# Kernel optimization log

Hardware: AMD Instinct MI355X
Metric: run time of the kernel (lower is better)

## Reference

```python
import jax, jax.numpy as jnp
import numpy as np

BN_EPS = 1e-5
BIND_CHAN = 4  # hparams.MODEL.LEARNABLE_OFFSET.BIND_CHAN


def conv1x1(x, w, b):
    # x: [B,C,H,W], w: [O,C], b: [O]
    return jnp.einsum('bchw,oc->bohw', x, w) + b[None, :, None, None]


def bn_train(x, gamma, beta):
    # training-mode batch norm over (B,H,W) per channel
    mean = jnp.mean(x, axis=(0, 2, 3), keepdims=True)
    var = jnp.var(x, axis=(0, 2, 3), keepdims=True)
    xn = (x - mean) * jax.lax.rsqrt(var + BN_EPS)
    return xn * gamma[None, :, None, None] + beta[None, :, None, None]


def displace_channel(x, offsets):
    # x: [B,C,H,W]; offsets: [C,2] (dy,dx) per channel, continuous.
    # out[b,c,y,x] = bilinear sample of x[b,c] at (y+dy_c, x+dx_c), zeros outside.
    B, C, H, W = x.shape
    dy, dx = offsets[:, 0], offsets[:, 1]
    fy, fx = jnp.floor(dy), jnp.floor(dx)
    wy, wx = dy - fy, dx - fx          # fractional weights, [C]
    iy, ix = fy.astype(jnp.int32), fx.astype(jnp.int32)
    chan = jnp.arange(C)[:, None, None]

    def shifted(oy, ox):
        ys = jnp.arange(H)[None, :] + oy[:, None]   # [C,H]
        xs = jnp.arange(W)[None, :] + ox[:, None]   # [C,W]
        valid = ((ys >= 0) & (ys < H))[:, :, None] & ((xs >= 0) & (xs < W))[:, None, :]
        ysc = jnp.clip(ys, 0, H - 1)
        xsc = jnp.clip(xs, 0, W - 1)
        g = x[:, chan, ysc[:, :, None], xsc[:, None, :]]   # [B,C,H,W]
        return g * valid.astype(x.dtype)[None]

    w00 = ((1 - wy) * (1 - wx))[None, :, None, None]
    w01 = ((1 - wy) * wx)[None, :, None, None]
    w10 = (wy * (1 - wx))[None, :, None, None]
    w11 = (wy * wx)[None, :, None, None]
    return (w00 * shifted(iy, ix) + w01 * shifted(iy, ix + 1)
            + w10 * shifted(iy + 1, ix) + w11 * shifted(iy + 1, ix + 1))


def setup_inputs() -> dict:
    key = jax.random.key(0)
    ks = jax.random.split(key, 12)
    B, Cin, H, W = 16, 64, 128, 128
    Cd, Cout = 128, 64
    n_off = Cd // BIND_CHAN  # 32
    s_in = 1.0 / np.sqrt(Cin)
    s_d = 1.0 / np.sqrt(Cd)
    return {
        'x': jax.random.normal(ks[0], (B, Cin, H, W), jnp.float32),
        'pre_w': jax.random.uniform(ks[1], (Cd, Cin), jnp.float32, -s_in, s_in),
        'pre_b': jax.random.uniform(ks[2], (Cd,), jnp.float32, -s_in, s_in),
        'post_w': jax.random.uniform(ks[3], (Cout, Cd), jnp.float32, -s_d, s_d),
        'post_b': jax.random.uniform(ks[4], (Cout,), jnp.float32, -s_d, s_d),
        'atten_w': jax.random.uniform(ks[5], (Cd, Cin), jnp.float32, -s_in, s_in),
        'atten_b': jax.random.uniform(ks[6], (Cd,), jnp.float32, -s_in, s_in),
        'atten_bn_g': jnp.ones((Cd,), jnp.float32),
        'atten_bn_b': jnp.zeros((Cd,), jnp.float32),
        'offsets': jax.random.normal(ks[7], (n_off, 2), jnp.float32) * 3.0,
        'bn_g': jnp.ones((Cout,), jnp.float32),
        'bn_b': jnp.zeros((Cout,), jnp.float32),
    }


def reference(x, pre_w, pre_b, post_w, post_b, atten_w, atten_b,
              atten_bn_g, atten_bn_b, offsets, bn_g, bn_b):
    # pre_offset conv1x1
    out_pre = conv1x1(x, pre_w, pre_b)                        # [B,Cd,H,W]
    # DisplaceChannel: each offset shared by BIND_CHAN consecutive channels
    off_per_chan = jnp.repeat(offsets, BIND_CHAN, axis=0)     # [Cd,2]
    out_dis = displace_channel(out_pre, off_per_chan)
    # Attention branch: conv1x1 -> BN -> Softplus -> SpaceNormalization
    a = conv1x1(x, atten_w, atten_b)
    a = bn_train(a, atten_bn_g, atten_bn_b)
    a = jax.nn.softplus(a)
    out_atten = a / jnp.sum(a, axis=(2, 3), keepdims=True)    # spatial normalization
    # post_offset conv1x1 on gated displaced features
    out_post = conv1x1(out_atten * out_dis, post_w, post_b)
    # residual (inplanes == outplanes, stride 1 -> no downsample) + BN + ReLU
    out_skip = x + out_post
    return jax.nn.relu(bn_train(out_skip, bn_g, bn_b))
```

## Files before the change

kernel.cpp:

```cpp
#include <hip/hip_runtime.h>

#define HWSZ   16384
#define CIN    64
#define CD     128
#define COUT   64
#define BN_EPS 1e-5f

typedef __attribute__((ext_vector_type(8))) short short8x;
typedef __attribute__((ext_vector_type(4))) float floatx4;

#define WS_WT1   0
#define WS_WTP   16384
#define WS_DISP  24576
#define WS_ASTAT 25344
#define WS_OSTAT 25600
#define WS_SPAT  25728
#define WS_BIG   32768
#define WS_TOTAL_BYTES ((size_t)(32768 + 16777216) * 4)

__device__ __forceinline__ unsigned short f2bf(float f) {
    unsigned int u = __float_as_uint(f);
    u += 0x7fff + ((u >> 16) & 1);
    return (unsigned short)(u >> 16);
}
__device__ __forceinline__ float bf2f(unsigned short s) {
    return __uint_as_float(((unsigned int)s) << 16);
}
__device__ __forceinline__ float softplus_fast(float x) {
    return fmaxf(x, 0.f) + __logf(1.f + __expf(-fabsf(x)));
}
__device__ __forceinline__ float block_reduce(float v, float* sc) {
    #pragma unroll
    for (int off = 32; off >= 1; off >>= 1) v += __shfl_xor(v, off, 64);
    int wv = threadIdx.x >> 6, ln = threadIdx.x & 63;
    if (ln == 0) sc[wv] = v;
    __syncthreads();
    float r = (threadIdx.x < 4) ? sc[threadIdx.x] : 0.f;
    r += __shfl_xor(r, 1, 64);
    r += __shfl_xor(r, 2, 64);
    return r;
}

__global__ __launch_bounds__(256) void prep_kernel(
        const float* __restrict__ pre_w, const float* __restrict__ atten_w,
        const float* __restrict__ post_w, const float* __restrict__ offsets,
        float* __restrict__ ws) {
    int tid = blockIdx.x * 256 + threadIdx.x;
    unsigned short* wAB = (unsigned short*)(ws + WS_WT1);
    unsigned short* wP  = (unsigned short*)(ws + WS_WTP);
    float* disp = ws + WS_DISP;
    if (tid < 16384) {
        int o = tid >> 6, c = tid & 63;
        float v = (o < 128) ? pre_w[o * 64 + c] : atten_w[(o - 128) * 64 + c];
        wAB[tid] = f2bf(v);
    } else if (tid < 24576) {
        int k = tid - 16384;
        int o = k >> 7, c = k & 127;
        wP[k] = f2bf(post_w[o * 128 + c]);
    } else if (tid < 24704) {
        int c = tid - 24576;
        float dy = offsets[(c >> 2) * 2 + 0];
        float dx = offsets[(c >> 2) * 2 + 1];
        float fy = floorf(dy), fx = floorf(dx);
        float wy = dy - fy, wx = dx - fx;
        float* d = disp + c * 6;
        d[0] = fy; d[1] = fx;
        d[2] = (1.f - wy) * (1.f - wx);
        d[3] = (1.f - wy) * wx;
        d[4] = wy * (1.f - wx);
        d[5] = wy * wx;
    }
}

__global__ __launch_bounds__(256) void conv_pre_mfma(
        const float* __restrict__ x, const unsigned short* __restrict__ wAB,
        const float* __restrict__ pre_b, const float* __restrict__ atten_b,
        unsigned short* __restrict__ out_pre, unsigned short* __restrict__ a_out) {
    __shared__ unsigned short xT[2][64 * 72];
    int t = threadIdx.x;
    int wv = t >> 6, ln = t & 63;
    int b = blockIdx.x >> 6;
    int poff = (blockIdx.x & 63) << 8;
    const float* xg = x + (size_t)b * CIN * HWSZ + poff;
    int c = ln;

    int o0 = wv * 64;
    short8x wfrag[4][2];
    #pragma unroll
    for (int oi = 0; oi < 4; ++oi)
        #pragma unroll
        for (int kk = 0; kk < 2; ++kk) {
            int row = o0 + oi * 16 + (ln & 15);
            int kcol = kk * 32 + (ln >> 4) * 8;
            wfrag[oi][kk] = *(const short8x*)(wAB + row * 64 + kcol);
        }
    float4 biasv[4];
    #pragma unroll
    for (int oi = 0; oi < 4; ++oi) {
        int og = o0 + oi * 16;
        const float* bias = (og < 128) ? (pre_b + og) : (atten_b + og - 128);
        biasv[oi] = *(const float4*)(bias + (ln >> 4) * 4);
    }

    float4 ld[4];
    #pragma unroll
    for (int k = 0; k < 4; ++k)
        ld[k] = *(const float4*)(xg + (size_t)c * HWSZ + 0 * 64 + wv * 16 + k * 4);
    #pragma unroll
    for (int k = 0; k < 4; ++k) {
        int px = wv * 16 + k * 4;
        xT[0][(px + 0) * 72 + c] = f2bf(ld[k].x);
        xT[0][(px + 1) * 72 + c] = f2bf(ld[k].y);
        xT[0][(px + 2) * 72 + c] = f2bf(ld[k].z);
        xT[0][(px + 3) * 72 + c] = f2bf(ld[k].w);
    }
    __syncthreads();

    #pragma unroll
    for (int tt = 0; tt < 4; ++tt) {
        if (tt < 3) {
            #pragma unroll
            for (int k = 0; k < 4; ++k)
                ld[k] = *(const float4*)(xg + (size_t)c * HWSZ + (tt + 1) * 64 + wv * 16 + k * 4);
        }
        const unsigned short* buf = xT[tt & 1];
        floatx4 acc[4][4];
        #pragma unroll
        for (int oi = 0; oi < 4; ++oi)
            #pragma unroll
            for (int pi = 0; pi < 4; ++pi)
                acc[oi][pi] = floatx4{biasv[oi].x, biasv[oi].y, biasv[oi].z, biasv[oi].w};
        #pragma unroll
        for (int kk = 0; kk < 2; ++kk)
            #pragma unroll
            for (int pi = 0; pi < 4; ++pi) {
                short8x xfrag = *(const short8x*)((const char*)buf +
                        (pi * 16 + (ln & 15)) * 144 + (kk * 32 + (ln >> 4) * 8) * 2);
                #pragma unroll
                for (int oi = 0; oi < 4; ++oi)
                    acc[oi][pi] = __builtin_amdgcn_mfma_f32_16x16x32_bf16(
                            wfrag[oi][kk], xfrag, acc[oi][pi], 0, 0, 0);
            }
        int ptile = poff + tt * 64;
        #pragma unroll
        for (int oi = 0; oi < 4; ++oi) {
            int og = o0 + oi * 16;
            unsigned short* dst = (og < 128) ? out_pre : a_out;
            int ob = (og < 128) ? og : og - 128;
            #pragma unroll
            for (int pi = 0; pi < 4; ++pi) {
                int px = ptile + pi * 16 + (ln & 15);
                #pragma unroll
                for (int r = 0; r < 4; ++r) {
                    int o = ob + (ln >> 4) * 4 + r;
                    dst[((size_t)b * CD + o) * HWSZ + px] = f2bf(acc[oi][pi][r]);
                }
            }
        }
        if (tt < 3) {
            unsigned short* wbuf = xT[(tt + 1) & 1];
            #pragma unroll
            for (int k = 0; k < 4; ++k) {
                int px = wv * 16 + k * 4;
                wbuf[(px + 0) * 72 + c] = f2bf(ld[k].x);
                wbuf[(px + 1) * 72 + c] = f2bf(ld[k].y);
                wbuf[(px + 2) * 72 + c] = f2bf(ld[k].z);
                wbuf[(px + 3) * 72 + c] = f2bf(ld[k].w);
            }
        }
        __syncthreads();
    }
}

__global__ __launch_bounds__(256) void chan_stats_bf16(
        const unsigned short* __restrict__ src, float* __restrict__ stats) {
    __shared__ float sc1[8], sc2[8];
    int c = blockIdx.x, b = blockIdx.y;
    const unsigned short* base = src + ((size_t)b * CD + c) * HWSZ;
    int t = threadIdx.x;
    float sum = 0.f, sq = 0.f;
    #pragma unroll
    for (int i = 0; i < 8; ++i) {
        uint4 v = *(const uint4*)(base + i * 2048 + t * 8);
        unsigned int u[4] = {v.x, v.y, v.z, v.w};
        #pragma unroll
        for (int k = 0; k < 4; ++k) {
            float lo = bf2f((unsigned short)(u[k] & 0xffff));
            float hi = bf2f((unsigned short)(u[k] >> 16));
            sum += lo + hi;
            sq  += lo * lo + hi * hi;
        }
    }
    sum = block_reduce(sum, sc1);
    __syncthreads();
    sq = block_reduce(sq, sc2);
    if (t == 0) {
        atomicAdd(&stats[c * 2 + 0], sum);
        atomicAdd(&stats[c * 2 + 1], sq);
    }
}

__global__ __launch_bounds__(256) void bn_softplus(
        unsigned int* __restrict__ a, const float* __restrict__ stats,
        const float* __restrict__ g, const float* __restrict__ bb,
        float* __restrict__ spat) {
    __shared__ float sc[8];
    int bc = blockIdx.x;
    int c = bc & 127;
    const float N = 262144.f;
    float mean = stats[c * 2] / N;
    float var  = stats[c * 2 + 1] / N - mean * mean;
    float rstd = rsqrtf(var + BN_EPS);
    float scl = rstd * g[c];
    float shf = bb[c] - mean * scl;
    unsigned int* base = a + (size_t)bc * (HWSZ / 2);
    int t = threadIdx.x;
    float lsum = 0.f;
    #pragma unroll 2
    for (int i = 0; i < 8; ++i) {
        uint4 v = *(uint4*)(base + i * 1024 + t * 4);
        unsigned int* u = (unsigned int*)&v;
        #pragma unroll
        for (int k = 0; k < 4; ++k) {
            float lo = bf2f((unsigned short)(u[k] & 0xffff));
            float hi = bf2f((unsigned short)(u[k] >> 16));
            lo = softplus_fast(lo * scl + shf);
            hi = softplus_fast(hi * scl + shf);
            lsum += lo + hi;
            u[k] = (unsigned int)f2bf(lo) | ((unsigned int)f2bf(hi) << 16);
        }
        *(uint4*)(base + i * 1024 + t * 4) = v;
    }
    lsum = block_reduce(lsum, sc);
    if (t == 0) spat[bc] = lsum;
}

struct Win9 { float v0,v1,v2,v3,v4,v5,v6,v7,v8; };
__device__ __forceinline__ Win9 extract9(uint4 qa, uint4 qb, bool s4, int sh) {
    unsigned long long A0 = ((unsigned long long)qa.y << 32) | qa.x;
    unsigned long long A1 = ((unsigned long long)qa.w << 32) | qa.z;
    unsigned long long A2 = ((unsigned long long)qb.y << 32) | qb.x;
    unsigned long long A3 = ((unsigned long long)qb.w << 32) | qb.z;
    unsigned long long B0 = s4 ? A1 : A0;
    unsigned long long B1 = s4 ? A2 : A1;
    unsigned long long B2 = s4 ? A3 : A2;
    unsigned long long r0 = sh ? ((B0 >> sh) | (B1 << (64 - sh))) : B0;
    unsigned long long r1 = sh ? ((B1 >> sh) | (B2 << (64 - sh))) : B1;
    unsigned int v8w = (unsigned int)(sh ? (B2 >> sh) : B2);
    Win9 w;
    w.v0 = bf2f((unsigned short)(r0 >>  0)); w.v1 = bf2f((unsigned short)(r0 >> 16));
    w.v2 = bf2f((unsigned short)(r0 >> 32)); w.v3 = bf2f((unsigned short)(r0 >> 48));
    w.v4 = bf2f((unsigned short)(r1 >>  0)); w.v5 = bf2f((unsigned short)(r1 >> 16));
    w.v6 = bf2f((unsigned short)(r1 >> 32)); w.v7 = bf2f((unsigned short)(r1 >> 48));
    w.v8 = bf2f((unsigned short)(v8w & 0xffff));
    return w;
}

__global__ __launch_bounds__(256) void displace_mul(
        unsigned short* __restrict__ pre, const unsigned short* __restrict__ a_sp,
        const float* __restrict__ spat, const float* __restrict__ disp) {
    __shared__ unsigned short img[128 * 136];
    int bc = blockIdx.x;
    int cc = bc & 127;
    const float* d = disp + cc * 6;
    int iy = (int)d[0], ix = (int)d[1];
    float w00 = d[2], w01 = d[3], w10 = d[4], w11 = d[5];
    float inv = 1.f / spat[bc];
    unsigned short* pb = pre + (size_t)bc * HWSZ;
    const unsigned short* ab = a_sp + (size_t)bc * HWSZ;
    int t = threadIdx.x;
    #pragma unroll
    for (int i = 0; i < 8; ++i) {
        int px = i * 2048 + t * 8;
        uint4 v = *(const uint4*)(pb + px);
        int y = px >> 7, xx = px & 127;
        *(uint4*)&img[y * 136 + xx] = v;
    }
    __syncthreads();
    int s = ix & 7;
    int ix8 = ix - s;
    int sh = (s & 3) * 16;
    bool s4 = s >= 4;
    for (int i = 0; i < 8; ++i) {
        int px = i * 2048 + t * 8;
        int y = px >> 7, x0 = px & 127;
        int yy0 = y + iy, yy1 = yy0 + 1;
        float wA0 = (yy0 >= 0 && yy0 < 128) ? w00 : 0.f;
        float wA1 = (yy0 >= 0 && yy0 < 128) ? w01 : 0.f;
        float wB0 = (yy1 >= 0 && yy1 < 128) ? w10 : 0.f;
        float wB1 = (yy1 >= 0 && yy1 < 128) ? w11 : 0.f;
        int yc0 = min(max(yy0, 0), 127), yc1 = min(max(yy1, 0), 127);
        int w0 = x0 + ix8;
        uint4 z = {0u, 0u, 0u, 0u};
        uint4 qa0 = (w0 >= 0 && w0 <= 120)         ? *(const uint4*)&img[yc0 * 136 + w0]     : z;
        uint4 qa1 = (w0 + 8 >= 0 && w0 + 8 <= 120) ? *(const uint4*)&img[yc0 * 136 + w0 + 8] : z;
        uint4 qb0 = (w0 >= 0 && w0 <= 120)         ? *(const uint4*)&img[yc1 * 136 + w0]     : z;
        uint4 qb1 = (w0 + 8 >= 0 && w0 + 8 <= 120) ? *(const uint4*)&img[yc1 * 136 + w0 + 8] : z;
        Win9 va = extract9(qa0, qa1, s4, sh);
        Win9 vb = extract9(qb0, qb1, s4, sh);
        float dv0 = wA0*va.v0 + wA1*va.v1 + wB0*vb.v0 + wB1*vb.v1;
        float dv1 = wA0*va.v1 + wA1*va.v2 + wB0*vb.v1 + wB1*vb.v2;
        float dv2 = wA0*va.v2 + wA1*va.v3 + wB0*vb.v2 + wB1*vb.v3;
        float dv3 = wA0*va.v3 + wA1*va.v4 + wB0*vb.v3 + wB1*vb.v4;
        float dv4 = wA0*va.v4 + wA1*va.v5 + wB0*vb.v4 + wB1*vb.v5;
        float dv5 = wA0*va.v5 + wA1*va.v6 + wB0*vb.v5 + wB1*vb.v6;
        float dv6 = wA0*va.v6 + wA1*va.v7 + wB0*vb.v6 + wB1*vb.v7;
        float dv7 = wA0*va.v7 + wA1*va.v8 + wB0*vb.v7 + wB1*vb.v8;
        uint4 av = *(const uint4*)(ab + px);
        unsigned int au[4] = {av.x, av.y, av.z, av.w};
        float a0 = bf2f((unsigned short)(au[0] & 0xffff)) * inv;
        float a1 = bf2f((unsigned short)(au[0] >> 16)) * inv;
        float a2 = bf2f((unsigned short)(au[1] & 0xffff)) * inv;
        float a3 = bf2f((unsigned short)(au[1] >> 16)) * inv;
        float a4 = bf2f((unsigned short)(au[2] & 0xffff)) * inv;
        float a5 = bf2f((unsigned short)(au[2] >> 16)) * inv;
        float a6 = bf2f((unsigned short)(au[3] & 0xffff)) * inv;
        float a7 = bf2f((unsigned short)(au[3] >> 16)) * inv;
        uint4 o;
        o.x = (unsigned int)f2bf(dv0 * a0) | ((unsigned int)f2bf(dv1 * a1) << 16);
        o.y = (unsigned int)f2bf(dv2 * a2) | ((unsigned int)f2bf(dv3 * a3) << 16);
        o.z = (unsigned int)f2bf(dv4 * a4) | ((unsigned int)f2bf(dv5 * a5) << 16);
        o.w = (unsigned int)f2bf(dv6 * a6) | ((unsigned int)f2bf(dv7 * a7) << 16);
        *(uint4*)(pb + px) = o;
    }
}

__global__ __launch_bounds__(256) void conv_post_mfma(
        const unsigned short* __restrict__ m, const unsigned short* __restrict__ wP,
        const float* __restrict__ post_b, const float* __restrict__ x,
        unsigned short* __restrict__ skipS) {
    __shared__ unsigned short mT[128 * 128];
    int t = threadIdx.x;
    int P0 = blockIdx.x * 128;
    int b = P0 >> 14, poff = P0 & 16383;
    int cl = t & 31, q = t >> 5;
    #pragma unroll
    for (int pass = 0; pass < 4; ++pass) {
        int c = cl + pass * 32;
        const unsigned short* mrow = m + ((size_t)b * CD + c) * HWSZ + poff;
        #pragma unroll
        for (int h = 0; h < 2; ++h) {
            int px0 = h * 64 + q * 8;
            uint4 v = *(const uint4*)(mrow + px0);
            unsigned int u[4] = {v.x, v.y, v.z, v.w};
            #pragma unroll
            for (int j = 0; j < 8; ++j) {
                unsigned short val = (unsigned short)((u[j >> 1] >> ((j & 1) * 16)) & 0xffff);
                int byteoff = (px0 + j) * 256 + ((c * 2) ^ (j << 4));
                *(unsigned short*)((char*)mT + byteoff) = val;
            }
        }
    }
    __syncthreads();
    int ln = t & 63, wv = t >> 6;
    int o0 = (wv >> 1) * 32;
    int ph = (wv & 1) * 64;
    short8x aw[2][4];
    #pragma unroll
    for (int oi = 0; oi < 2; ++oi)
        #pragma unroll
        for (int kk = 0; kk < 4; ++kk)
            aw[oi][kk] = *(const short8x*)(wP + (o0 + oi * 16 + (ln & 15)) * 128 + kk * 32 + (ln >> 4) * 8);
    floatx4 acc[2][4];
    #pragma unroll
    for (int oi = 0; oi < 2; ++oi)
        #pragma unroll
        for (int pi = 0; pi < 4; ++pi) acc[oi][pi] = floatx4{0.f, 0.f, 0.f, 0.f};
    #pragma unroll
    for (int kk = 0; kk < 4; ++kk)
        #pragma unroll
        for (int pi = 0; pi < 4; ++pi) {
            int px = ph + pi * 16 + (ln & 15);
            int cb = kk * 64 + (ln >> 4) * 16;
            short8x bf = *(const short8x*)((const char*)mT + px * 256 + (cb ^ ((px & 7) << 4)));
            #pragma unroll
            for (int oi = 0; oi < 2; ++oi)
                acc[oi][pi] = __builtin_amdgcn_mfma_f32_16x16x32_bf16(aw[oi][kk], bf, acc[oi][pi], 0, 0, 0);
        }
    #pragma unroll
    for (int oi = 0; oi < 2; ++oi) {
        float4 b4 = *(const float4*)(post_b + o0 + oi * 16 + (ln >> 4) * 4);
        float bb[4] = {b4.x, b4.y, b4.z, b4.w};
        #pragma unroll
        for (int pi = 0; pi < 4; ++pi) {
            int pxg = poff + ph + pi * 16 + (ln & 15);
            #pragma unroll
            for (int r = 0; r < 4; ++r) {
                int o = o0 + oi * 16 + (ln >> 4) * 4 + r;
                float val = acc[oi][pi][r] + bb[r] + x[((size_t)b * COUT + o) * HWSZ + pxg];
                skipS[((size_t)b * CD + o) * HWSZ + pxg] = f2bf(val);
            }
        }
    }
}

__global__ __launch_bounds__(256) void bn_relu_out(
        const unsigned short* __restrict__ skipS, float* __restrict__ out,
        const float* __restrict__ stats, const float* __restrict__ g,
        const float* __restrict__ bb) {
    const float N = 262144.f;
    int t = threadIdx.x;
    #pragma unroll
    for (int k = 0; k < 4; ++k) {
        size_t gidx = (size_t)blockIdx.x * 1024 + k * 256 + t;
        size_t e = gidx * 8;
        int b = (int)(e >> 20);
        int c = (int)(e >> 14) & 63;
        int px = (int)(e & 16383);
        float mean = stats[c * 2] / N;
        float rstd = rsqrtf(stats[c * 2 + 1] / N - mean * mean + BN_EPS);
        float gc = g[c], bbc = bb[c];
        uint4 v = *(const uint4*)(skipS + ((size_t)b * CD + c) * HWSZ + px);
        unsigned int u[4] = {v.x, v.y, v.z, v.w};
        float4 o0, o1;
        float* op[8] = {&o0.x, &o0.y, &o0.z, &o0.w, &o1.x, &o1.y, &o1.z, &o1.w};
        #pragma unroll
        for (int j = 0; j < 8; ++j) {
            float val = bf2f((unsigned short)((u[j >> 1] >> ((j & 1) * 16)) & 0xffff));
            *op[j] = fmaxf((val - mean) * rstd * gc + bbc, 0.f);
        }
        *(float4*)(out + e) = o0;
        *(float4*)(out + e + 4) = o1;
    }
}

extern "C" void kernel_launch(void* const* d_in, const int* in_sizes, int n_in,
                              void* d_out, int out_size, void* d_ws, size_t ws_size,
                              hipStream_t stream) {
    const float* x          = (const float*)d_in[0];
    const float* pre_w      = (const float*)d_in[1];
    const float* pre_b      = (const float*)d_in[2];
    const float* post_w     = (const float*)d_in[3];
    const float* post_b     = (const float*)d_in[4];
    const float* atten_w    = (const float*)d_in[5];
    const float* atten_b    = (const float*)d_in[6];
    const float* atten_bn_g = (const float*)d_in[7];
    const float* atten_bn_b = (const float*)d_in[8];
    const float* offsets    = (const float*)d_in[9];
    const float* bn_g       = (const float*)d_in[10];
    const float* bn_b       = (const float*)d_in[11];
    float* out = (float*)d_out;
    float* ws  = (float*)d_ws;

    if (ws_size < WS_TOTAL_BYTES) return;

    unsigned short* wAB = (unsigned short*)(ws + WS_WT1);
    unsigned short* wP  = (unsigned short*)(ws + WS_WTP);
    float* disp    = ws + WS_DISP;
    float* a_stats = ws + WS_ASTAT;
    float* o_stats = ws + WS_OSTAT;
    float* spat    = ws + WS_SPAT;
    unsigned short* big   = (unsigned short*)(ws + WS_BIG);
    unsigned short* a_buf = (unsigned short*)d_out;

    hipMemsetAsync((void*)a_stats, 0, 384 * sizeof(float), stream);

    prep_kernel<<<97, 256, 0, stream>>>(pre_w, atten_w, post_w, offsets, ws);
    conv_pre_mfma<<<1024, 256, 0, stream>>>(x, wAB, pre_b, atten_b, big, a_buf);
    chan_stats_bf16<<<dim3(128, 16), 256, 0, stream>>>(a_buf, a_stats);
    bn_softplus<<<2048, 256, 0, stream>>>((unsigned int*)a_buf, a_stats, atten_bn_g, atten_bn_b, spat);
    displace_mul<<<2048, 256, 0, stream>>>(big, a_buf, spat, disp);
    conv_post_mfma<<<2048, 256, 0, stream>>>(big, wP, post_b, x, big);
    chan_stats_bf16<<<dim3(64, 16), 256, 0, stream>>>(big, o_stats);
    bn_relu_out<<<2048, 256, 0, stream>>>(big, out, o_stats, bn_g, bn_b);
}
```

Baseline: 180.1 us.

## Fuse BN-softplus and spatial sum into displace kernel; deepen conv_pre prefetch

Removes the separate bn_softplus kernel. The displace kernel now applies BN, softplus and the spatial-sum reduction to the raw attention tile and keeps the result in LDS, which drops one full read-modify-write pass over the attention buffer plus one launch. The cost is roughly 32KB more LDS per block (img plus asp), which may reduce occupancy. Separately, conv_pre is unrolled by hand with two register prefetch buffers, so global loads run two tiles ahead of compute.

New measurement: 175.3 us. 1.03x faster.

```diff
diff --git a/kernel.cpp b/kernel.cpp
--- a/kernel.cpp
+++ b/kernel.cpp
@@ -14,7 +14,6 @@
 #define WS_DISP  24576
 #define WS_ASTAT 25344
 #define WS_OSTAT 25600
-#define WS_SPAT  25728
 #define WS_BIG   32768
 #define WS_TOTAL_BYTES ((size_t)(32768 + 16777216) * 4)
 
@@ -72,6 +71,56 @@
     }
 }
 
+__device__ __forceinline__ void pre_write_lds(unsigned short* wbuf, int c, int wv,
+                                              const float4 ld[4]) {
+    #pragma unroll
+    for (int k = 0; k < 4; ++k) {
+        int px = wv * 16 + k * 4;
+        wbuf[(px + 0) * 72 + c] = f2bf(ld[k].x);
+        wbuf[(px + 1) * 72 + c] = f2bf(ld[k].y);
+        wbuf[(px + 2) * 72 + c] = f2bf(ld[k].z);
+        wbuf[(px + 3) * 72 + c] = f2bf(ld[k].w);
+    }
+}
+
+__device__ __forceinline__ void pre_compute_tile(
+        const unsigned short* buf, int ln, int o0, int b, int ptile,
+        const short8x wfrag[4][2], const float4 biasv[4],
+        unsigned short* __restrict__ out_pre, unsigned short* __restrict__ a_out) {
+    floatx4 acc[4][4];
+    #pragma unroll
+    for (int oi = 0; oi < 4; ++oi)
+        #pragma unroll
+        for (int pi = 0; pi < 4; ++pi)
+            acc[oi][pi] = floatx4{biasv[oi].x, biasv[oi].y, biasv[oi].z, biasv[oi].w};
+    #pragma unroll
+    for (int kk = 0; kk < 2; ++kk)
+        #pragma unroll
+        for (int pi = 0; pi < 4; ++pi) {
+            short8x xfrag = *(const short8x*)((const char*)buf +
+                    (pi * 16 + (ln & 15)) * 144 + (kk * 32 + (ln >> 4) * 8) * 2);
+            #pragma unroll
+            for (int oi = 0; oi < 4; ++oi)
+                acc[oi][pi] = __builtin_amdgcn_mfma_f32_16x16x32_bf16(
+                        wfrag[oi][kk], xfrag, acc[oi][pi], 0, 0, 0);
+        }
+    #pragma unroll
+    for (int oi = 0; oi < 4; ++oi) {
+        int og = o0 + oi * 16;
+        unsigned short* dst = (og < 128) ? out_pre : a_out;
+        int ob = (og < 128) ? og : og - 128;
+        #pragma unroll
+        for (int pi = 0; pi < 4; ++pi) {
+            int px = ptile + pi * 16 + (ln & 15);
+            #pragma unroll
+            for (int r = 0; r < 4; ++r) {
+                int o = ob + (ln >> 4) * 4 + r;
+                dst[((size_t)b * CD + o) * HWSZ + px] = f2bf(acc[oi][pi][r]);
+            }
+        }
+    }
+}
+
 __global__ __launch_bounds__(256) void conv_pre_mfma(
         const float* __restrict__ x, const unsigned short* __restrict__ wAB,
         const float* __restrict__ pre_b, const float* __restrict__ atten_b,
@@ -102,74 +151,35 @@
         biasv[oi] = *(const float4*)(bias + (ln >> 4) * 4);
     }
 
-    float4 ld[4];
+    float4 lda[4], ldb[4];
     #pragma unroll
     for (int k = 0; k < 4; ++k)
-        ld[k] = *(const float4*)(xg + (size_t)c * HWSZ + 0 * 64 + wv * 16 + k * 4);
-    #pragma unroll
-    for (int k = 0; k < 4; ++k) {
-        int px = wv * 16 + k * 4;
-        xT[0][(px + 0) * 72 + c] = f2bf(ld[k].x);
-        xT[0][(px + 1) * 72 + c] = f2bf(ld[k].y);
-        xT[0][(px + 2) * 72 + c] = f2bf(ld[k].z);
-        xT[0][(px + 3) * 72 + c] = f2bf(ld[k].w);
-    }
-    __syncthreads();
-
-    #pragma unroll
-    for (int tt = 0; tt < 4; ++tt) {
-        if (tt < 3) {
-            #pragma unroll
-            for (int k = 0; k < 4; ++k)
-                ld[k] = *(const float4*)(xg + (size_t)c * HWSZ + (tt + 1) * 64 + wv * 16 + k * 4);
-        }
-        const unsigned short* buf = xT[tt & 1];
-        floatx4 acc[4][4];
-        #pragma unroll
-        for (int oi = 0; oi < 4; ++oi)
-            #pragma unroll
-            for (int pi = 0; pi < 4; ++pi)
-                acc[oi][pi] = floatx4{biasv[oi].x, biasv[oi].y, biasv[oi].z, biasv[oi].w};
-        #pragma unroll
-        for (int kk = 0; kk < 2; ++kk)
-            #pragma unroll
-            for (int pi = 0; pi < 4; ++pi) {
-                short8x xfrag = *(const short8x*)((const char*)buf +
-                        (pi * 16 + (ln & 15)) * 144 + (kk * 32 + (ln >> 4) * 8) * 2);
-                #pragma unroll
-                for (int oi = 0; oi < 4; ++oi)
-                    acc[oi][pi] = __builtin_amdgcn_mfma_f32_16x16x32_bf16(
-                            wfrag[oi][kk], xfrag, acc[oi][pi], 0, 0, 0);
-            }
-        int ptile = poff + tt * 64;
-        #pragma unroll
-        for (int oi = 0; oi < 4; ++oi) {
-            int og = o0 + oi * 16;
-            unsigned short* dst = (og < 128) ? out_pre : a_out;
-            int ob = (og < 128) ? og : og - 128;
-            #pragma unroll
-            for (int pi = 0; pi < 4; ++pi) {
-                int px = ptile + pi * 16 + (ln & 15);
-                #pragma unroll
-                for (int r = 0; r < 4; ++r) {
-                    int o = ob + (ln >> 4) * 4 + r;
-                    dst[((size_t)b * CD + o) * HWSZ + px] = f2bf(acc[oi][pi][r]);
-                }
-            }
-        }
-        if (tt < 3) {
-            unsigned short* wbuf = xT[(tt + 1) & 1];
-            #pragma unroll
-            for (int k = 0; k < 4; ++k) {
-                int px = wv * 16 + k * 4;
-                wbuf[(px + 0) * 72 + c] = f2bf(ld[k].x);
-                wbuf[(px + 1) * 72 + c] = f2bf(ld[k].y);
-                wbuf[(px + 2) * 72 + c] = f2bf(ld[k].z);
-                wbuf[(px + 3) * 72 + c] = f2bf(ld[k].w);
-            }
-        }
-        __syncthreads();
-    }
+        lda[k] = *(const float4*)(xg + (size_t)c * HWSZ + 0 * 64 + wv * 16 + k * 4);
+    pre_write_lds(xT[0], c, wv, lda);
+    #pragma unroll
+    for (int k = 0; k < 4; ++k)
+        lda[k] = *(const float4*)(xg + (size_t)c * HWSZ + 1 * 64 + wv * 16 + k * 4);
+    __syncthreads();
+
+    #pragma unroll
+    for (int k = 0; k < 4; ++k)
+        ldb[k] = *(const float4*)(xg + (size_t)c * HWSZ + 2 * 64 + wv * 16 + k * 4);
+    pre_compute_tile(xT[0], ln, o0, b, poff + 0 * 64, wfrag, biasv, out_pre, a_out);
+    pre_write_lds(xT[1], c, wv, lda);
+    __syncthreads();
+
+    #pragma unroll
+    for (int k = 0; k < 4; ++k)
+        lda[k] = *(const float4*)(xg + (size_t)c * HWSZ + 3 * 64 + wv * 16 + k * 4);
+    pre_compute_tile(xT[1], ln, o0, b, poff + 1 * 64, wfrag, biasv, out_pre, a_out);
+    pre_write_lds(xT[0], c, wv, ldb);
+    __syncthreads();
+
+    pre_compute_tile(xT[0], ln, o0, b, poff + 2 * 64, wfrag, biasv, out_pre, a_out);
+    pre_write_lds(xT[1], c, wv, lda);
+    __syncthreads();
+
+    pre_compute_tile(xT[1], ln, o0, b, poff + 3 * 64, wfrag, biasv, out_pre, a_out);
 }
 
 __global__ __launch_bounds__(256) void chan_stats_bf16(
@@ -198,41 +208,6 @@
         atomicAdd(&stats[c * 2 + 0], sum);
         atomicAdd(&stats[c * 2 + 1], sq);
     }
-}
-
-__global__ __launch_bounds__(256) void bn_softplus(
-        unsigned int* __restrict__ a, const float* __restrict__ stats,
-        const float* __restrict__ g, const float* __restrict__ bb,
-        float* __restrict__ spat) {
-    __shared__ float sc[8];
-    int bc = blockIdx.x;
-    int c = bc & 127;
-    const float N = 262144.f;
-    float mean = stats[c * 2] / N;
-    float var  = stats[c * 2 + 1] / N - mean * mean;
-    float rstd = rsqrtf(var + BN_EPS);
-    float scl = rstd * g[c];
-    float shf = bb[c] - mean * scl;
-    unsigned int* base = a + (size_t)bc * (HWSZ / 2);
-    int t = threadIdx.x;
-    float lsum = 0.f;
-    #pragma unroll 2
-    for (int i = 0; i < 8; ++i) {
-        uint4 v = *(uint4*)(base + i * 1024 + t * 4);
-        unsigned int* u = (unsigned int*)&v;
-        #pragma unroll
-        for (int k = 0; k < 4; ++k) {
-            float lo = bf2f((unsigned short)(u[k] & 0xffff));
-            float hi = bf2f((unsigned short)(u[k] >> 16));
-            lo = softplus_fast(lo * scl + shf);
-            hi = softplus_fast(hi * scl + shf);
-            lsum += lo + hi;
-            u[k] = (unsigned int)f2bf(lo) | ((unsigned int)f2bf(hi) << 16);
-        }
-        *(uint4*)(base + i * 1024 + t * 4) = v;
-    }
-    lsum = block_reduce(lsum, sc);
-    if (t == 0) spat[bc] = lsum;
 }
 
 struct Win9 { float v0,v1,v2,v3,v4,v5,v6,v7,v8; };
@@ -256,27 +231,52 @@
     return w;
 }
 
-__global__ __launch_bounds__(256) void displace_mul(
-        unsigned short* __restrict__ pre, const unsigned short* __restrict__ a_sp,
-        const float* __restrict__ spat, const float* __restrict__ disp) {
+__global__ __launch_bounds__(256) void displace_bnsp_mul(
+        unsigned short* __restrict__ pre, const unsigned short* __restrict__ a_raw,
+        const float* __restrict__ stats, const float* __restrict__ g,
+        const float* __restrict__ bb, const float* __restrict__ disp) {
     __shared__ unsigned short img[128 * 136];
+    __shared__ unsigned short asp[16384];
+    __shared__ float sc[8];
+    __shared__ float s_inv;
     int bc = blockIdx.x;
     int cc = bc & 127;
     const float* d = disp + cc * 6;
     int iy = (int)d[0], ix = (int)d[1];
     float w00 = d[2], w01 = d[3], w10 = d[4], w11 = d[5];
-    float inv = 1.f / spat[bc];
+    const float N = 262144.f;
+    float mean = stats[cc * 2] / N;
+    float var  = stats[cc * 2 + 1] / N - mean * mean;
+    float rstd = rsqrtf(var + BN_EPS);
+    float scl = rstd * g[cc];
+    float shf = bb[cc] - mean * scl;
     unsigned short* pb = pre + (size_t)bc * HWSZ;
-    const unsigned short* ab = a_sp + (size_t)bc * HWSZ;
+    const unsigned short* ab = a_raw + (size_t)bc * HWSZ;
     int t = threadIdx.x;
+    float lsum = 0.f;
     #pragma unroll
     for (int i = 0; i < 8; ++i) {
         int px = i * 2048 + t * 8;
         uint4 v = *(const uint4*)(pb + px);
         int y = px >> 7, xx = px & 127;
         *(uint4*)&img[y * 136 + xx] = v;
-    }
-    __syncthreads();
+        uint4 av = *(const uint4*)(ab + px);
+        unsigned int au[4] = {av.x, av.y, av.z, av.w};
+        uint4 o;
+        unsigned int* ou = (unsigned int*)&o;
+        #pragma unroll
+        for (int k = 0; k < 4; ++k) {
+            float lo = softplus_fast(bf2f((unsigned short)(au[k] & 0xffff)) * scl + shf);
+            float hi = softplus_fast(bf2f((unsigned short)(au[k] >> 16))    * scl + shf);
+            lsum += lo + hi;
+            ou[k] = (unsigned int)f2bf(lo) | ((unsigned int)f2bf(hi) << 16);
+        }
+        *(uint4*)&asp[px] = o;
+    }
+    lsum = block_reduce(lsum, sc);
+    if (t == 0) s_inv = 1.f / lsum;
+    __syncthreads();
+    float inv = s_inv;
     int s = ix & 7;
     int ix8 = ix - s;
     int sh = (s & 3) * 16;
@@ -306,7 +306,7 @@
         float dv5 = wA0*va.v5 + wA1*va.v6 + wB0*vb.v5 + wB1*vb.v6;
         float dv6 = wA0*va.v6 + wA1*va.v7 + wB0*vb.v6 + wB1*vb.v7;
         float dv7 = wA0*va.v7 + wA1*va.v8 + wB0*vb.v7 + wB1*vb.v8;
-        uint4 av = *(const uint4*)(ab + px);
+        uint4 av = *(const uint4*)&asp[px];
         unsigned int au[4] = {av.x, av.y, av.z, av.w};
         float a0 = bf2f((unsigned short)(au[0] & 0xffff)) * inv;
         float a1 = bf2f((unsigned short)(au[0] >> 16)) * inv;
@@ -449,7 +449,6 @@
     float* disp    = ws + WS_DISP;
     float* a_stats = ws + WS_ASTAT;
     float* o_stats = ws + WS_OSTAT;
-    float* spat    = ws + WS_SPAT;
     unsigned short* big   = (unsigned short*)(ws + WS_BIG);
     unsigned short* a_buf = (unsigned short*)d_out;
 
@@ -458,8 +457,7 @@
     prep_kernel<<<97, 256, 0, stream>>>(pre_w, atten_w, post_w, offsets, ws);
     conv_pre_mfma<<<1024, 256, 0, stream>>>(x, wAB, pre_b, atten_b, big, a_buf);
     chan_stats_bf16<<<dim3(128, 16), 256, 0, stream>>>(a_buf, a_stats);
-    bn_softplus<<<2048, 256, 0, stream>>>((unsigned int*)a_buf, a_stats, atten_bn_g, atten_bn_b, spat);
-    displace_mul<<<2048, 256, 0, stream>>>(big, a_buf, spat, disp);
+    displace_bnsp_mul<<<2048, 256, 0, stream>>>(big, a_buf, a_stats, atten_bn_g, atten_bn_b, disp);
     conv_post_mfma<<<2048, 256, 0, stream>>>(big, wP, post_b, x, big);
     chan_stats_bf16<<<dim3(64, 16), 256, 0, stream>>>(big, o_stats);
     bn_relu_out<<<2048, 256, 0, stream>>>(big, out, o_stats, bn_g, bn_b);
```
